# Kernel tuning notes

Measured on AMD Instinct MI355X. Metric: run time of the kernel, lower is better.

## Reference

```python
import jax, jax.numpy as jnp
import numpy as np

N_NODES = 50000
EPS = 1e-5


def setup_inputs() -> dict:
    key = jax.random.key(0)
    ks = jax.random.split(key, 8)
    B, N, F, H = 2, N_NODES, 128, 128
    E = 800000
    x = jax.random.normal(ks[0], (B, N, F), dtype=jnp.float32)
    edge_index = jax.random.randint(ks[1], (2, E), 0, N, dtype=jnp.int32)
    # Xavier-uniform weights, zero biases (matches reset_parameters)
    def xavier(k, fin, fout):
        lim = np.sqrt(6.0 / (fin + fout)).astype(np.float32)
        return jax.random.uniform(k, (fin, fout), jnp.float32, -lim, lim)
    return {
        "x": x,
        "edge_index": edge_index,
        "W1": xavier(ks[2], F, H), "b1": jnp.zeros((H,), jnp.float32),
        "W2": xavier(ks[3], H, H), "b2": jnp.zeros((H,), jnp.float32),
        "W3": xavier(ks[4], H, 1), "b3": jnp.zeros((1,), jnp.float32),
        "gamma1": jnp.ones((H,), jnp.float32), "beta1": jnp.zeros((H,), jnp.float32),
        "gamma2": jnp.ones((H,), jnp.float32), "beta2": jnp.zeros((H,), jnp.float32),
    }


def _gconv(h, edge_index, W, b):
    # h: [B, N, Fin] -> support: [B, N, Fout]
    sup = jnp.einsum('bnf,fo->bno', h, W)
    row, col = edge_index[0], edge_index[1]
    # gather source rows, scatter-add into destination rows (per batch, vmapped)
    agg = jax.vmap(lambda s: jax.ops.segment_sum(s[row], col, num_segments=N_NODES))(sup)
    return agg + b


def _bn(h, gamma, beta):
    # BatchNorm1d over flattened (B*N, F): training-mode batch statistics
    m = jnp.mean(h, axis=(0, 1))
    v = jnp.var(h, axis=(0, 1))
    return (h - m) * jax.lax.rsqrt(v + EPS) * gamma + beta


def reference(x, edge_index, W1, b1, W2, b2, W3, b3, gamma1, beta1, gamma2, beta2):
    h = _gconv(x, edge_index, W1, b1)
    h = jax.nn.relu(_bn(h, gamma1, beta1))
    h = _gconv(h, edge_index, W2, b2)
    h = jax.nn.relu(_bn(h, gamma2, beta2))
    out = _gconv(h, edge_index, W3, b3)
    return out[..., 0]  # squeeze(-1) -> [B, N]
```

## Files before the change

### kernel.cpp

```cpp
#include <hip/hip_runtime.h>

#define N_NODES 50000
#define N_EDGES 800000
#define FDIM 128
#define NROWS 100000
#define BN_EPS 1e-5f
#define CAP 64
#define NREP 64

typedef unsigned short ushort_t;
typedef unsigned int uint_t;
typedef __attribute__((ext_vector_type(8))) short bf16x8;
typedef __attribute__((ext_vector_type(4))) float f32x4;

__device__ inline ushort_t f2bf(float f) {
    uint_t x = __float_as_uint(f);
    x += 0x7fffu + ((x >> 16) & 1u);
    return (ushort_t)(x >> 16);
}
__device__ inline float4 bf4_to_f4(ushort4 u) {
    float4 f;
    f.x = __uint_as_float((uint_t)u.x << 16);
    f.y = __uint_as_float((uint_t)u.y << 16);
    f.z = __uint_as_float((uint_t)u.z << 16);
    f.w = __uint_as_float((uint_t)u.w << 16);
    return f;
}
__device__ inline void round4(float4 v, bf16x8& hi, int base) {
    hi[base + 0] = (short)f2bf(v.x);
    hi[base + 1] = (short)f2bf(v.y);
    hi[base + 2] = (short)f2bf(v.z);
    hi[base + 3] = (short)f2bf(v.w);
}

__global__ __launch_bounds__(256) void wsplit_kernel(const float* __restrict__ W1,
                                                     const float* __restrict__ W2,
                                                     ushort_t* __restrict__ wt,
                                                     int* __restrict__ cnt,
                                                     float* __restrict__ stats) {
    int idx = blockIdx.x * 256 + threadIdx.x;
    for (int i = idx; i < N_NODES; i += 32768) cnt[i] = 0;
    stats[idx] = 0.f;
    int which = idx >> 14;
    int e = idx & 16383;
    int k = e >> 7, n = e & 127;
    float f = (which ? W2 : W1)[e];
    ushort_t h = f2bf(f);
    float fh = __uint_as_float((uint_t)h << 16);
    ushort_t l = f2bf(f - fh);
    size_t base = (size_t)which * 32768;
    wt[base + n * 128 + k] = h;
    wt[base + 16384 + n * 128 + k] = l;
}

__global__ __launch_bounds__(256) void bucket_kernel(const int* __restrict__ row,
                                                     const int* __restrict__ col,
                                                     int* __restrict__ cnt,
                                                     int* __restrict__ srcbuf) {
    int e = blockIdx.x * 256 + threadIdx.x;
    if (e < N_EDGES) {
        int c = col[e];
        int p = atomicAdd(&cnt[c], 1);
        if (p < CAP) srcbuf[(c << 6) + p] = row[e];
    }
}

template <bool BN>
__global__ __launch_bounds__(256) void gemm_mfma2(const float* __restrict__ A,
                                                  const ushort_t* __restrict__ wt,
                                                  const float* __restrict__ stats,
                                                  const float* __restrict__ gamma,
                                                  const float* __restrict__ beta,
                                                  ushort_t* __restrict__ C) {
    __shared__ short lds[24576];
    __shared__ float cs[256];
    int tid = threadIdx.x;
    long r0 = (long)blockIdx.x * 64;
    const float4* A4 = (const float4*)A;

    if (BN) {
        if (tid < 128) {
            float s = 0.f, s2 = 0.f;
            for (int r = 0; r < NREP; ++r) {
                s  += stats[r * 256 + tid];
                s2 += stats[r * 256 + 128 + tid];
            }
            float inv = 1.0f / (float)NROWS;
            float mean = s * inv;
            float var = s2 * inv - mean * mean;
            float scale = gamma[tid] / sqrtf(var + BN_EPS);
            cs[tid] = scale;
            cs[128 + tid] = beta[tid] - mean * scale;
        }
        __syncthreads();
    }
    const float4* coef4 = (const float4*)cs;

    #pragma unroll
    for (int i = 0; i < 4; ++i) {
        int li = tid + i * 256;
        int r = li >> 4, j = li & 15;
        long gr = r0 + r;
        float4 va = make_float4(0.f, 0.f, 0.f, 0.f), vb = va;
        if (gr < NROWS) { va = A4[gr * 32 + j * 2]; vb = A4[gr * 32 + j * 2 + 1]; }
        if (BN) {
            float4 sc = coef4[j * 2], sh = coef4[32 + j * 2];
            va.x = fmaxf(va.x * sc.x + sh.x, 0.f);
            va.y = fmaxf(va.y * sc.y + sh.y, 0.f);
            va.z = fmaxf(va.z * sc.z + sh.z, 0.f);
            va.w = fmaxf(va.w * sc.w + sh.w, 0.f);
            sc = coef4[j * 2 + 1]; sh = coef4[32 + j * 2 + 1];
            vb.x = fmaxf(vb.x * sc.x + sh.x, 0.f);
            vb.y = fmaxf(vb.y * sc.y + sh.y, 0.f);
            vb.z = fmaxf(vb.z * sc.z + sh.z, 0.f);
            vb.w = fmaxf(vb.w * sc.w + sh.w, 0.f);
        }
        bf16x8 vh;
        round4(va, vh, 0);
        round4(vb, vh, 4);
        *(bf16x8*)&lds[r * 128 + ((j ^ (r & 15)) * 8)] = vh;
    }

    int w = tid >> 6, l = tid & 63;
    int m = l & 15, q = l >> 4;
    for (int half = 0; half < 2; ++half) {
        __syncthreads();
        #pragma unroll
        for (int i = 0; i < 8; ++i) {
            int li = tid + i * 256;
            int p = li >> 10;
            int rest = li & 1023;
            int nl = rest >> 4, j = rest & 15;
            bf16x8 v = *(const bf16x8*)&wt[(size_t)p * 16384 + (half * 64 + nl) * 128 + j * 8];
            *(bf16x8*)&lds[8192 + p * 8192 + nl * 128 + ((j ^ (nl & 15)) * 8)] = v;
        }
        __syncthreads();

        f32x4 acc[4] = {};
        #pragma unroll
        for (int s = 0; s < 4; ++s) {
            int x = (s * 4 + q) ^ m;
            bf16x8 ah = *(const bf16x8*)&lds[(w * 16 + m) * 128 + x * 8];
            #pragma unroll
            for (int c = 0; c < 4; ++c) {
                int boff = 8192 + (c * 16 + m) * 128 + x * 8;
                bf16x8 bh = *(const bf16x8*)&lds[boff];
                bf16x8 bl = *(const bf16x8*)&lds[8192 + boff];
                acc[c] = __builtin_amdgcn_mfma_f32_16x16x32_bf16(ah, bl, acc[c], 0, 0, 0);
                acc[c] = __builtin_amdgcn_mfma_f32_16x16x32_bf16(ah, bh, acc[c], 0, 0, 0);
            }
        }

        #pragma unroll
        for (int c = 0; c < 4; ++c) {
            #pragma unroll
            for (int r = 0; r < 4; ++r) {
                long gr = r0 + w * 16 + q * 4 + r;
                if (gr < NROWS) {
                    int b = gr >= N_NODES;
                    long node = gr - (long)b * N_NODES;
                    C[(node * 2 + b) * 128 + half * 64 + c * 16 + m] = f2bf(acc[c][r]);
                }
            }
        }
    }
}

__global__ __launch_bounds__(256) void aggregate_bf16(const ushort_t* __restrict__ sup,
                                                      const int* __restrict__ cnt,
                                                      const int* __restrict__ srcbuf,
                                                      float* __restrict__ agg,
                                                      float* __restrict__ stats) {
    __shared__ float lsb[4][256];
    int lane = threadIdx.x & 63;
    int wid = threadIdx.x >> 6;
    int node = blockIdx.x * 4 + wid;
    int s = lane >> 5;
    int l32 = lane & 31;
    int m = cnt[node]; if (m > CAP) m = CAP;
    const ushort4* sb = (const ushort4*)sup;
    float4 a0 = make_float4(0.f, 0.f, 0.f, 0.f);
    float4 a1 = make_float4(0.f, 0.f, 0.f, 0.f);
    int idx = (lane < m) ? srcbuf[(node << 6) + lane] : 0;
    int tmax = (m + 1) >> 1;
    #pragma unroll 2
    for (int t = 0; t < tmax; ++t) {
        int j = 2 * t + s;
        int r = __shfl(idx, j & 63);
        ushort4 u0 = sb[(size_t)r * 64 + l32];
        ushort4 u1 = sb[(size_t)r * 64 + 32 + l32];
        if (j < m) {
            float4 f0 = bf4_to_f4(u0);
            float4 f1 = bf4_to_f4(u1);
            a0.x += f0.x; a0.y += f0.y; a0.z += f0.z; a0.w += f0.w;
            a1.x += f1.x; a1.y += f1.y; a1.z += f1.z; a1.w += f1.w;
        }
    }
    a0.x += __shfl_xor(a0.x, 32); a0.y += __shfl_xor(a0.y, 32);
    a0.z += __shfl_xor(a0.z, 32); a0.w += __shfl_xor(a0.w, 32);
    a1.x += __shfl_xor(a1.x, 32); a1.y += __shfl_xor(a1.y, 32);
    a1.z += __shfl_xor(a1.z, 32); a1.w += __shfl_xor(a1.w, 32);
    float4* ag = (float4*)agg;
    if (s == 0) {
        ag[(size_t)node * 32 + l32] = a0;
        lsb[wid][l32 * 8 + 0] = a0.x + a1.x;
        lsb[wid][l32 * 8 + 1] = a0.y + a1.y;
        lsb[wid][l32 * 8 + 2] = a0.z + a1.z;
        lsb[wid][l32 * 8 + 3] = a0.w + a1.w;
        lsb[wid][l32 * 8 + 4] = a0.x * a0.x + a1.x * a1.x;
        lsb[wid][l32 * 8 + 5] = a0.y * a0.y + a1.y * a1.y;
        lsb[wid][l32 * 8 + 6] = a0.z * a0.z + a1.z * a1.z;
        lsb[wid][l32 * 8 + 7] = a0.w * a0.w + a1.w * a1.w;
    } else {
        ag[(size_t)(N_NODES + node) * 32 + l32] = a1;
    }
    __syncthreads();
    int tid = threadIdx.x;
    float v = lsb[0][tid] + lsb[1][tid] + lsb[2][tid] + lsb[3][tid];
    int f = (tid >> 3) * 4 + (tid & 3);
    int isq = (tid >> 2) & 1;
    atomicAdd(&stats[(blockIdx.x & (NREP - 1)) * 256 + isq * 128 + f], v);
}

__global__ __launch_bounds__(256) void gemv_bn_kernel(const float* __restrict__ h,
                                                      const float* __restrict__ stats,
                                                      const float* __restrict__ gamma,
                                                      const float* __restrict__ beta,
                                                      const float* __restrict__ W3,
                                                      float* __restrict__ sup3) {
    __shared__ float cs[256];
    int tid = threadIdx.x;
    if (tid < 128) {
        float s = 0.f, s2 = 0.f;
        for (int r = 0; r < NREP; ++r) {
            s  += stats[r * 256 + tid];
            s2 += stats[r * 256 + 128 + tid];
        }
        float inv = 1.0f / (float)NROWS;
        float mean = s * inv;
        float var = s2 * inv - mean * mean;
        float scale = gamma[tid] / sqrtf(var + BN_EPS);
        cs[tid] = scale;
        cs[128 + tid] = beta[tid] - mean * scale;
    }
    __syncthreads();
    int lane = tid & 63, wid = tid >> 6;
    float2 w  = ((const float2*)W3)[lane];
    float2 sc = ((const float2*)cs)[lane];
    float2 sh = ((const float2*)(cs + 128))[lane];
    #pragma unroll
    for (int r = 0; r < 4; ++r) {
        long gw = (long)blockIdx.x * 16 + wid * 4 + r;
        float2 v = ((const float2*)h)[(size_t)gw * 64 + lane];
        v.x = fmaxf(v.x * sc.x + sh.x, 0.f);
        v.y = fmaxf(v.y * sc.y + sh.y, 0.f);
        float s = v.x * w.x + v.y * w.y;
        #pragma unroll
        for (int d = 32; d > 0; d >>= 1) s += __shfl_xor(s, d);
        if (lane == 0) sup3[gw] = s;
    }
}

__global__ __launch_bounds__(256) void gather_out_kernel(const int* __restrict__ cnt,
                                                         const int* __restrict__ srcbuf,
                                                         const float* __restrict__ sup3,
                                                         const float* __restrict__ b3,
                                                         float* __restrict__ out) {
    int n = blockIdx.x * 256 + threadIdx.x;
    if (n >= N_NODES) return;
    int m = cnt[n]; if (m > CAP) m = CAP;
    int base = n << 6;
    float s0 = 0.f, s1 = 0.f;
    for (int i = 0; i < m; ++i) {
        int r = srcbuf[base + i];
        s0 += sup3[r];
        s1 += sup3[N_NODES + r];
    }
    float b = b3[0];
    out[n] = s0 + b;
    out[N_NODES + n] = s1 + b;
}


extern "C" void kernel_launch(void* const* d_in, const int* in_sizes, int n_in,
                              void* d_out, int out_size, void* d_ws, size_t ws_size,
                              hipStream_t stream) {
    const float* x      = (const float*)d_in[0];
    const int*   ei     = (const int*)d_in[1];
    const float* W1     = (const float*)d_in[2];
    const float* W2     = (const float*)d_in[4];
    const float* W3     = (const float*)d_in[6];
    const float* b3     = (const float*)d_in[7];
    const float* gamma1 = (const float*)d_in[8];
    const float* beta1  = (const float*)d_in[9];
    const float* gamma2 = (const float*)d_in[10];
    const float* beta2  = (const float*)d_in[11];
    const int* rowp = ei;
    const int* colp = ei + N_EDGES;

    ushort_t* sup   = (ushort_t*)d_ws;
    float* agg      = (float*)(sup + 12800000);
    float* sup3     = agg + 12800000;
    ushort_t* wt    = (ushort_t*)(sup3 + 100000);
    float* stats    = (float*)(wt + 65536);
    int*   cnt      = (int*)(stats + 32768);
    int*   srcbuf   = cnt + N_NODES;
    float* out      = (float*)d_out;

    wsplit_kernel  <<<128,   256, 0, stream>>>(W1, W2, wt, cnt, stats);
    bucket_kernel  <<<3125,  256, 0, stream>>>(rowp, colp, cnt, srcbuf);

    gemm_mfma2<false><<<1563,  256, 0, stream>>>(x, wt, nullptr, nullptr, nullptr, sup);
    aggregate_bf16   <<<12500, 256, 0, stream>>>(sup, cnt, srcbuf, agg, stats);

    gemm_mfma2<true> <<<1563,  256, 0, stream>>>(agg, wt + 32768, stats, gamma1, beta1, sup);
    aggregate_bf16   <<<12500, 256, 0, stream>>>(sup, cnt, srcbuf, agg, stats + 16384);

    gemv_bn_kernel   <<<6250, 256, 0, stream>>>(agg, stats + 16384, gamma2, beta2, W3, sup3);
    gather_out_kernel<<<196,  256, 0, stream>>>(cnt, srcbuf, sup3, b3, out);
}
```

Baseline: 359.1 us.

## Slice support features into 16-column planes for cache-local aggregation, shrink indices to u16

The GEMM now writes the bf16 support matrix as eight feature-slice planes of 16 columns each, instead of one 128-wide row per node. Each aggregation block handles one slice for 32 nodes, so the gathered working set per slice (about 3.2 MB) can stay cache resident rather than scattering 256-byte rows across the whole 25 MB table. Source indices are stored as 16-bit values to halve index traffic, and agg and index accesses use nontemporal hints. The cost is eight times more index reads and loop overhead per node, narrower 64-byte gathers, and a per-slice stats reduction.

```diff
diff --git a/kernel.cpp b/kernel.cpp
--- a/kernel.cpp
+++ b/kernel.cpp
@@ -12,19 +12,12 @@
 typedef unsigned int uint_t;
 typedef __attribute__((ext_vector_type(8))) short bf16x8;
 typedef __attribute__((ext_vector_type(4))) float f32x4;
+typedef __attribute__((ext_vector_type(2))) float f32x2;
 
 __device__ inline ushort_t f2bf(float f) {
     uint_t x = __float_as_uint(f);
     x += 0x7fffu + ((x >> 16) & 1u);
     return (ushort_t)(x >> 16);
-}
-__device__ inline float4 bf4_to_f4(ushort4 u) {
-    float4 f;
-    f.x = __uint_as_float((uint_t)u.x << 16);
-    f.y = __uint_as_float((uint_t)u.y << 16);
-    f.z = __uint_as_float((uint_t)u.z << 16);
-    f.w = __uint_as_float((uint_t)u.w << 16);
-    return f;
 }
 __device__ inline void round4(float4 v, bf16x8& hi, int base) {
     hi[base + 0] = (short)f2bf(v.x);
@@ -56,12 +49,12 @@
 __global__ __launch_bounds__(256) void bucket_kernel(const int* __restrict__ row,
                                                      const int* __restrict__ col,
                                                      int* __restrict__ cnt,
-                                                     int* __restrict__ srcbuf) {
+                                                     ushort_t* __restrict__ srcbuf) {
     int e = blockIdx.x * 256 + threadIdx.x;
     if (e < N_EDGES) {
         int c = col[e];
         int p = atomicAdd(&cnt[c], 1);
-        if (p < CAP) srcbuf[(c << 6) + p] = row[e];
+        if (p < CAP) srcbuf[(c << 6) + p] = (ushort_t)row[e];
     }
 }
 
@@ -159,7 +152,8 @@
                 if (gr < NROWS) {
                     int b = gr >= N_NODES;
                     long node = gr - (long)b * N_NODES;
-                    C[(node * 2 + b) * 128 + half * 64 + c * 16 + m] = f2bf(acc[c][r]);
+                    C[((size_t)(half * 4 + c) * (N_NODES * 2) + node * 2 + b) * 16 + m] =
+                        f2bf(acc[c][r]);
                 }
             }
         }
@@ -168,58 +162,76 @@
 
 __global__ __launch_bounds__(256) void aggregate_bf16(const ushort_t* __restrict__ sup,
                                                       const int* __restrict__ cnt,
-                                                      const int* __restrict__ srcbuf,
+                                                      const ushort_t* __restrict__ srcbuf,
                                                       float* __restrict__ agg,
                                                       float* __restrict__ stats) {
-    __shared__ float lsb[4][256];
-    int lane = threadIdx.x & 63;
-    int wid = threadIdx.x >> 6;
-    int node = blockIdx.x * 4 + wid;
-    int s = lane >> 5;
-    int l32 = lane & 31;
-    int m = cnt[node]; if (m > CAP) m = CAP;
-    const ushort4* sb = (const ushort4*)sup;
-    float4 a0 = make_float4(0.f, 0.f, 0.f, 0.f);
-    float4 a1 = make_float4(0.f, 0.f, 0.f, 0.f);
-    int idx = (lane < m) ? srcbuf[(node << 6) + lane] : 0;
-    int tmax = (m + 1) >> 1;
-    #pragma unroll 2
-    for (int t = 0; t < tmax; ++t) {
-        int j = 2 * t + s;
-        int r = __shfl(idx, j & 63);
-        ushort4 u0 = sb[(size_t)r * 64 + l32];
-        ushort4 u1 = sb[(size_t)r * 64 + 32 + l32];
-        if (j < m) {
-            float4 f0 = bf4_to_f4(u0);
-            float4 f1 = bf4_to_f4(u1);
-            a0.x += f0.x; a0.y += f0.y; a0.z += f0.z; a0.w += f0.w;
-            a1.x += f1.x; a1.y += f1.y; a1.z += f1.z; a1.w += f1.w;
-        }
-    }
-    a0.x += __shfl_xor(a0.x, 32); a0.y += __shfl_xor(a0.y, 32);
-    a0.z += __shfl_xor(a0.z, 32); a0.w += __shfl_xor(a0.w, 32);
-    a1.x += __shfl_xor(a1.x, 32); a1.y += __shfl_xor(a1.y, 32);
-    a1.z += __shfl_xor(a1.z, 32); a1.w += __shfl_xor(a1.w, 32);
-    float4* ag = (float4*)agg;
-    if (s == 0) {
-        ag[(size_t)node * 32 + l32] = a0;
-        lsb[wid][l32 * 8 + 0] = a0.x + a1.x;
-        lsb[wid][l32 * 8 + 1] = a0.y + a1.y;
-        lsb[wid][l32 * 8 + 2] = a0.z + a1.z;
-        lsb[wid][l32 * 8 + 3] = a0.w + a1.w;
-        lsb[wid][l32 * 8 + 4] = a0.x * a0.x + a1.x * a1.x;
-        lsb[wid][l32 * 8 + 5] = a0.y * a0.y + a1.y * a1.y;
-        lsb[wid][l32 * 8 + 6] = a0.z * a0.z + a1.z * a1.z;
-        lsb[wid][l32 * 8 + 7] = a0.w * a0.w + a1.w * a1.w;
-    } else {
-        ag[(size_t)(N_NODES + node) * 32 + l32] = a1;
+    __shared__ float lst[2][4][16];
+    int tid = threadIdx.x;
+    int lane = tid & 63, wid = tid >> 6;
+    int slice = blockIdx.x & 7;
+    int g = blockIdx.x >> 3;
+    int base_node = g * 32 + wid * 8;
+    int sub = lane & 15, eg = lane >> 4;
+    int b = sub >> 3, fpair = sub & 7;
+    const uint_t* supu = (const uint_t*)sup + (size_t)slice * N_NODES * 16;
+    f32x2* agg2 = (f32x2*)agg;
+
+    int mv = 0;
+    if (lane < 8 && base_node + lane < N_NODES) {
+        mv = cnt[base_node + lane];
+        if (mv > CAP) mv = CAP;
+    }
+    int idxv[8];
+    #pragma unroll
+    for (int k = 0; k < 8; ++k) {
+        int node = base_node + k;
+        int mk = __shfl(mv, k);
+        idxv[k] = (node < N_NODES && lane < mk)
+                    ? (int)__builtin_nontemporal_load(&srcbuf[((size_t)node << 6) + lane])
+                    : 0;
+    }
+
+    f32x2 ssum = {0.f, 0.f}, ssq = {0.f, 0.f};
+    #pragma unroll
+    for (int k = 0; k < 8; ++k) {
+        int node = base_node + k;
+        if (node < N_NODES) {
+            int mk = __shfl(mv, k);
+            float ax = 0.f, ay = 0.f;
+            int tmax = (mk + 3) >> 2;
+            #pragma unroll 2
+            for (int t = 0; t < tmax; ++t) {
+                int j = t * 4 + eg;
+                int r = __shfl(idxv[k], j & 63);
+                uint_t u = supu[(size_t)r * 16 + sub];
+                if (j < mk) {
+                    ax += __uint_as_float(u << 16);
+                    ay += __uint_as_float(u & 0xffff0000u);
+                }
+            }
+            ax += __shfl_xor(ax, 16); ay += __shfl_xor(ay, 16);
+            ax += __shfl_xor(ax, 32); ay += __shfl_xor(ay, 32);
+            if (lane < 16) {
+                size_t row = (size_t)b * N_NODES + node;
+                f32x2 v2 = {ax, ay};
+                __builtin_nontemporal_store(v2, &agg2[row * 64 + slice * 8 + fpair]);
+            }
+            float ox = __shfl_xor(ax, 8), oy = __shfl_xor(ay, 8);
+            ssum.x += ax + ox;           ssum.y += ay + oy;
+            ssq.x  += ax * ax + ox * ox; ssq.y  += ay * ay + oy * oy;
+        }
+    }
+    if (lane < 8) {
+        lst[0][wid][fpair * 2] = ssum.x; lst[0][wid][fpair * 2 + 1] = ssum.y;
+        lst[1][wid][fpair * 2] = ssq.x;  lst[1][wid][fpair * 2 + 1] = ssq.y;
     }
     __syncthreads();
-    int tid = threadIdx.x;
-    float v = lsb[0][tid] + lsb[1][tid] + lsb[2][tid] + lsb[3][tid];
-    int f = (tid >> 3) * 4 + (tid & 3);
-    int isq = (tid >> 2) & 1;
-    atomicAdd(&stats[(blockIdx.x & (NREP - 1)) * 256 + isq * 128 + f], v);
+    if (tid < 32) {
+        int which = tid >> 4, f = tid & 15;
+        float v = lst[which][0][f] + lst[which][1][f] + lst[which][2][f] + lst[which][3][f];
+        int rep = (blockIdx.x >> 3) & (NREP - 1);
+        atomicAdd(&stats[rep * 256 + which * 128 + slice * 16 + f], v);
+    }
 }
 
 __global__ __launch_bounds__(256) void gemv_bn_kernel(const float* __restrict__ h,
@@ -262,7 +274,7 @@
 }
 
 __global__ __launch_bounds__(256) void gather_out_kernel(const int* __restrict__ cnt,
-                                                         const int* __restrict__ srcbuf,
+                                                         const ushort_t* __restrict__ srcbuf,
                                                          const float* __restrict__ sup3,
                                                          const float* __restrict__ b3,
                                                          float* __restrict__ out) {
@@ -304,17 +316,17 @@
     ushort_t* wt    = (ushort_t*)(sup3 + 100000);
     float* stats    = (float*)(wt + 65536);
     int*   cnt      = (int*)(stats + 32768);
-    int*   srcbuf   = cnt + N_NODES;
+    ushort_t* srcbuf = (ushort_t*)(cnt + N_NODES);
     float* out      = (float*)d_out;
 
     wsplit_kernel  <<<128,   256, 0, stream>>>(W1, W2, wt, cnt, stats);
     bucket_kernel  <<<3125,  256, 0, stream>>>(rowp, colp, cnt, srcbuf);
 
     gemm_mfma2<false><<<1563,  256, 0, stream>>>(x, wt, nullptr, nullptr, nullptr, sup);
-    aggregate_bf16   <<<12500, 256, 0, stream>>>(sup, cnt, srcbuf, agg, stats);
+    aggregate_bf16   <<<12504, 256, 0, stream>>>(sup, cnt, srcbuf, agg, stats);
 
     gemm_mfma2<true> <<<1563,  256, 0, stream>>>(agg, wt + 32768, stats, gamma1, beta1, sup);
-    aggregate_bf16   <<<12500, 256, 0, stream>>>(sup, cnt, srcbuf, agg, stats + 16384);
+    aggregate_bf16   <<<12504, 256, 0, stream>>>(sup, cnt, srcbuf, agg, stats + 16384);
 
     gemv_bn_kernel   <<<6250, 256, 0, stream>>>(agg, stats + 16384, gamma2, beta2, W3, sup3);
     gather_out_kernel<<<196,  256, 0, stream>>>(cnt, srcbuf, sup3, b3, out);
```

After: 538.5 us. +49.9%, slower.

## Fuse init/bucket/gemm and gemv/gather into cooperative persistent kernels

Applied to the files above, without the earlier changes.

Merges the weight-split/init, edge bucketing and first GEMM into one cooperative kernel, using a grid sync after init. It likewise merges the final GEMV and output gather into a second cooperative kernel with a grid sync between them. Phases become grid-stride loops over persistent blocks, and the old separate launches remain as a fallback if the cooperative launch fails. The aim is to cut launch overhead and inter-kernel gaps, at the cost of grid.sync and fewer resident blocks for the GEMM phase.

```diff
diff --git a/kernel.cpp b/kernel.cpp
--- a/kernel.cpp
+++ b/kernel.cpp
@@ -1,12 +1,16 @@
 #include <hip/hip_runtime.h>
+#include <hip/hip_cooperative_groups.h>
+
+namespace cg = cooperative_groups;
 
 #define N_NODES 50000
 #define N_EDGES 800000
-#define FDIM 128
 #define NROWS 100000
 #define BN_EPS 1e-5f
 #define CAP 64
 #define NREP 64
+#define HEAD_BLOCKS 768
+#define TAIL_BLOCKS 1024
 
 typedef unsigned short ushort_t;
 typedef unsigned int uint_t;
@@ -33,51 +37,48 @@
     hi[base + 3] = (short)f2bf(v.w);
 }
 
-__global__ __launch_bounds__(256) void wsplit_kernel(const float* __restrict__ W1,
-                                                     const float* __restrict__ W2,
-                                                     ushort_t* __restrict__ wt,
-                                                     int* __restrict__ cnt,
-                                                     float* __restrict__ stats) {
-    int idx = blockIdx.x * 256 + threadIdx.x;
-    for (int i = idx; i < N_NODES; i += 32768) cnt[i] = 0;
-    stats[idx] = 0.f;
-    int which = idx >> 14;
-    int e = idx & 16383;
-    int k = e >> 7, n = e & 127;
-    float f = (which ? W2 : W1)[e];
-    ushort_t h = f2bf(f);
-    float fh = __uint_as_float((uint_t)h << 16);
-    ushort_t l = f2bf(f - fh);
-    size_t base = (size_t)which * 32768;
-    wt[base + n * 128 + k] = h;
-    wt[base + 16384 + n * 128 + k] = l;
-}
-
-__global__ __launch_bounds__(256) void bucket_kernel(const int* __restrict__ row,
-                                                     const int* __restrict__ col,
-                                                     int* __restrict__ cnt,
-                                                     int* __restrict__ srcbuf) {
-    int e = blockIdx.x * 256 + threadIdx.x;
-    if (e < N_EDGES) {
-        int c = col[e];
+__device__ __forceinline__ void phase_init(const float* __restrict__ W1,
+                                           const float* __restrict__ W2,
+                                           ushort_t* __restrict__ wt,
+                                           int* __restrict__ cnt,
+                                           float* __restrict__ stats,
+                                           int gtid, int gsz) {
+    for (int i = gtid; i < N_NODES; i += gsz) cnt[i] = 0;
+    if (gtid < 32768) {
+        stats[gtid] = 0.f;
+        int which = gtid >> 14;
+        int e = gtid & 16383;
+        int k = e >> 7, n = e & 127;
+        float f = (which ? W2 : W1)[e];
+        ushort_t h = f2bf(f);
+        float fh = __uint_as_float((uint_t)h << 16);
+        ushort_t l = f2bf(f - fh);
+        size_t base = (size_t)which * 32768;
+        wt[base + n * 128 + k] = h;
+        wt[base + 16384 + n * 128 + k] = l;
+    }
+}
+
+__device__ __forceinline__ void phase_bucket(const int* __restrict__ rowp,
+                                             const int* __restrict__ colp,
+                                             int* __restrict__ cnt,
+                                             int* __restrict__ srcbuf,
+                                             int gtid, int gsz) {
+    for (int e = gtid; e < N_EDGES; e += gsz) {
+        int c = colp[e];
         int p = atomicAdd(&cnt[c], 1);
-        if (p < CAP) srcbuf[(c << 6) + p] = row[e];
+        if (p < CAP) srcbuf[(c << 6) + p] = rowp[e];
     }
 }
 
 template <bool BN>
-__global__ __launch_bounds__(256) void gemm_mfma2(const float* __restrict__ A,
-                                                  const ushort_t* __restrict__ wt,
-                                                  const float* __restrict__ stats,
-                                                  const float* __restrict__ gamma,
-                                                  const float* __restrict__ beta,
-                                                  ushort_t* __restrict__ C) {
-    __shared__ short lds[24576];
-    __shared__ float cs[256];
-    int tid = threadIdx.x;
-    long r0 = (long)blockIdx.x * 64;
-    const float4* A4 = (const float4*)A;
-
+__device__ __forceinline__ void phase_gemm(const float* __restrict__ A,
+                                           const ushort_t* __restrict__ wt,
+                                           const float* __restrict__ stats,
+                                           const float* __restrict__ gamma,
+                                           const float* __restrict__ beta,
+                                           ushort_t* __restrict__ C,
+                                           short* lds, float* cs, int tid) {
     if (BN) {
         if (tid < 128) {
             float s = 0.f, s2 = 0.f;
@@ -92,78 +93,206 @@
             cs[tid] = scale;
             cs[128 + tid] = beta[tid] - mean * scale;
         }
-        __syncthreads();
-    }
+    }
+    const float4* A4 = (const float4*)A;
     const float4* coef4 = (const float4*)cs;
-
-    #pragma unroll
-    for (int i = 0; i < 4; ++i) {
-        int li = tid + i * 256;
-        int r = li >> 4, j = li & 15;
-        long gr = r0 + r;
-        float4 va = make_float4(0.f, 0.f, 0.f, 0.f), vb = va;
-        if (gr < NROWS) { va = A4[gr * 32 + j * 2]; vb = A4[gr * 32 + j * 2 + 1]; }
-        if (BN) {
-            float4 sc = coef4[j * 2], sh = coef4[32 + j * 2];
-            va.x = fmaxf(va.x * sc.x + sh.x, 0.f);
-            va.y = fmaxf(va.y * sc.y + sh.y, 0.f);
-            va.z = fmaxf(va.z * sc.z + sh.z, 0.f);
-            va.w = fmaxf(va.w * sc.w + sh.w, 0.f);
-            sc = coef4[j * 2 + 1]; sh = coef4[32 + j * 2 + 1];
-            vb.x = fmaxf(vb.x * sc.x + sh.x, 0.f);
-            vb.y = fmaxf(vb.y * sc.y + sh.y, 0.f);
-            vb.z = fmaxf(vb.z * sc.z + sh.z, 0.f);
-            vb.w = fmaxf(vb.w * sc.w + sh.w, 0.f);
-        }
-        bf16x8 vh;
-        round4(va, vh, 0);
-        round4(vb, vh, 4);
-        *(bf16x8*)&lds[r * 128 + ((j ^ (r & 15)) * 8)] = vh;
-    }
-
     int w = tid >> 6, l = tid & 63;
     int m = l & 15, q = l >> 4;
-    for (int half = 0; half < 2; ++half) {
+
+    for (int tile = blockIdx.x; tile < 1563; tile += gridDim.x) {
         __syncthreads();
+        long r0 = (long)tile * 64;
         #pragma unroll
-        for (int i = 0; i < 8; ++i) {
+        for (int i = 0; i < 4; ++i) {
             int li = tid + i * 256;
-            int p = li >> 10;
-            int rest = li & 1023;
-            int nl = rest >> 4, j = rest & 15;
-            bf16x8 v = *(const bf16x8*)&wt[(size_t)p * 16384 + (half * 64 + nl) * 128 + j * 8];
-            *(bf16x8*)&lds[8192 + p * 8192 + nl * 128 + ((j ^ (nl & 15)) * 8)] = v;
-        }
-        __syncthreads();
-
-        f32x4 acc[4] = {};
-        #pragma unroll
-        for (int s = 0; s < 4; ++s) {
-            int x = (s * 4 + q) ^ m;
-            bf16x8 ah = *(const bf16x8*)&lds[(w * 16 + m) * 128 + x * 8];
+            int r = li >> 4, j = li & 15;
+            long gr = r0 + r;
+            float4 va = make_float4(0.f, 0.f, 0.f, 0.f), vb = va;
+            if (gr < NROWS) { va = A4[gr * 32 + j * 2]; vb = A4[gr * 32 + j * 2 + 1]; }
+            if (BN) {
+                float4 sc = coef4[j * 2], sh = coef4[32 + j * 2];
+                va.x = fmaxf(va.x * sc.x + sh.x, 0.f);
+                va.y = fmaxf(va.y * sc.y + sh.y, 0.f);
+                va.z = fmaxf(va.z * sc.z + sh.z, 0.f);
+                va.w = fmaxf(va.w * sc.w + sh.w, 0.f);
+                sc = coef4[j * 2 + 1]; sh = coef4[32 + j * 2 + 1];
+                vb.x = fmaxf(vb.x * sc.x + sh.x, 0.f);
+                vb.y = fmaxf(vb.y * sc.y + sh.y, 0.f);
+                vb.z = fmaxf(vb.z * sc.z + sh.z, 0.f);
+                vb.w = fmaxf(vb.w * sc.w + sh.w, 0.f);
+            }
+            bf16x8 vh;
+            round4(va, vh, 0);
+            round4(vb, vh, 4);
+            *(bf16x8*)&lds[r * 128 + ((j ^ (r & 15)) * 8)] = vh;
+        }
+        for (int half = 0; half < 2; ++half) {
+            __syncthreads();
+            #pragma unroll
+            for (int i = 0; i < 8; ++i) {
+                int li = tid + i * 256;
+                int p = li >> 10;
+                int rest = li & 1023;
+                int nl = rest >> 4, j = rest & 15;
+                bf16x8 v = *(const bf16x8*)&wt[(size_t)p * 16384 + (half * 64 + nl) * 128 + j * 8];
+                *(bf16x8*)&lds[8192 + p * 8192 + nl * 128 + ((j ^ (nl & 15)) * 8)] = v;
+            }
+            __syncthreads();
+
+            f32x4 acc[4] = {};
+            #pragma unroll
+            for (int s = 0; s < 4; ++s) {
+                int x = (s * 4 + q) ^ m;
+                bf16x8 ah = *(const bf16x8*)&lds[(w * 16 + m) * 128 + x * 8];
+                #pragma unroll
+                for (int c = 0; c < 4; ++c) {
+                    int boff = 8192 + (c * 16 + m) * 128 + x * 8;
+                    bf16x8 bh = *(const bf16x8*)&lds[boff];
+                    bf16x8 bl = *(const bf16x8*)&lds[8192 + boff];
+                    acc[c] = __builtin_amdgcn_mfma_f32_16x16x32_bf16(ah, bl, acc[c], 0, 0, 0);
+                    acc[c] = __builtin_amdgcn_mfma_f32_16x16x32_bf16(ah, bh, acc[c], 0, 0, 0);
+                }
+            }
             #pragma unroll
             for (int c = 0; c < 4; ++c) {
-                int boff = 8192 + (c * 16 + m) * 128 + x * 8;
-                bf16x8 bh = *(const bf16x8*)&lds[boff];
-                bf16x8 bl = *(const bf16x8*)&lds[8192 + boff];
-                acc[c] = __builtin_amdgcn_mfma_f32_16x16x32_bf16(ah, bl, acc[c], 0, 0, 0);
-                acc[c] = __builtin_amdgcn_mfma_f32_16x16x32_bf16(ah, bh, acc[c], 0, 0, 0);
-            }
-        }
-
-        #pragma unroll
-        for (int c = 0; c < 4; ++c) {
-            #pragma unroll
-            for (int r = 0; r < 4; ++r) {
-                long gr = r0 + w * 16 + q * 4 + r;
-                if (gr < NROWS) {
-                    int b = gr >= N_NODES;
-                    long node = gr - (long)b * N_NODES;
-                    C[(node * 2 + b) * 128 + half * 64 + c * 16 + m] = f2bf(acc[c][r]);
+                #pragma unroll
+                for (int r = 0; r < 4; ++r) {
+                    long gr = r0 + w * 16 + q * 4 + r;
+                    if (gr < NROWS) {
+                        int b = gr >= N_NODES;
+                        long node = gr - (long)b * N_NODES;
+                        C[(node * 2 + b) * 128 + half * 64 + c * 16 + m] = f2bf(acc[c][r]);
+                    }
                 }
             }
         }
     }
+}
+
+__device__ __forceinline__ void phase_gemv(const float* __restrict__ h,
+                                           const float* __restrict__ stats,
+                                           const float* __restrict__ gamma,
+                                           const float* __restrict__ beta,
+                                           const float* __restrict__ W3,
+                                           float* __restrict__ sup3,
+                                           float* cs, int tid) {
+    if (tid < 128) {
+        float s = 0.f, s2 = 0.f;
+        for (int r = 0; r < NREP; ++r) {
+            s  += stats[r * 256 + tid];
+            s2 += stats[r * 256 + 128 + tid];
+        }
+        float inv = 1.0f / (float)NROWS;
+        float mean = s * inv;
+        float var = s2 * inv - mean * mean;
+        float scale = gamma[tid] / sqrtf(var + BN_EPS);
+        cs[tid] = scale;
+        cs[128 + tid] = beta[tid] - mean * scale;
+    }
+    __syncthreads();
+    int lane = tid & 63, wid = tid >> 6;
+    float2 w  = ((const float2*)W3)[lane];
+    float2 sc = ((const float2*)cs)[lane];
+    float2 sh = ((const float2*)(cs + 128))[lane];
+    for (int g = blockIdx.x; g < 6250; g += gridDim.x) {
+        #pragma unroll
+        for (int r = 0; r < 4; ++r) {
+            long gw = (long)g * 16 + wid * 4 + r;
+            float2 v = ((const float2*)h)[(size_t)gw * 64 + lane];
+            v.x = fmaxf(v.x * sc.x + sh.x, 0.f);
+            v.y = fmaxf(v.y * sc.y + sh.y, 0.f);
+            float s = v.x * w.x + v.y * w.y;
+            #pragma unroll
+            for (int d = 32; d > 0; d >>= 1) s += __shfl_xor(s, d);
+            if (lane == 0) sup3[gw] = s;
+        }
+    }
+}
+
+__device__ __forceinline__ void phase_gather(const int* __restrict__ cnt,
+                                             const int* __restrict__ srcbuf,
+                                             const float* __restrict__ sup3,
+                                             const float* __restrict__ b3,
+                                             float* __restrict__ out,
+                                             int gtid, int gsz) {
+    for (int n = gtid; n < N_NODES; n += gsz) {
+        int m = cnt[n]; if (m > CAP) m = CAP;
+        int base = n << 6;
+        float s0 = 0.f, s1 = 0.f;
+        for (int i = 0; i < m; ++i) {
+            int r = srcbuf[base + i];
+            s0 += sup3[r];
+            s1 += sup3[N_NODES + r];
+        }
+        float b = b3[0];
+        out[n] = s0 + b;
+        out[N_NODES + n] = s1 + b;
+    }
+}
+
+__global__ __launch_bounds__(256, 3) void fused_head(const float* __restrict__ x,
+        const int* __restrict__ ei,
+        const float* __restrict__ W1, const float* __restrict__ W2,
+        ushort_t* __restrict__ wt, int* __restrict__ cnt,
+        float* __restrict__ stats, int* __restrict__ srcbuf,
+        ushort_t* __restrict__ sup) {
+    __shared__ short lds[24576];
+    __shared__ float cs[256];
+    cg::grid_group grid = cg::this_grid();
+    int tid = threadIdx.x;
+    int gtid = blockIdx.x * 256 + tid;
+    int gsz = gridDim.x * 256;
+    phase_init(W1, W2, wt, cnt, stats, gtid, gsz);
+    grid.sync();
+    phase_bucket(ei, ei + N_EDGES, cnt, srcbuf, gtid, gsz);
+    phase_gemm<false>(x, wt, nullptr, nullptr, nullptr, sup, lds, cs, tid);
+}
+
+__global__ __launch_bounds__(256, 4) void fused_tail(const float* __restrict__ h,
+        const float* __restrict__ stats,
+        const float* __restrict__ gamma, const float* __restrict__ beta,
+        const float* __restrict__ W3, const float* __restrict__ b3,
+        float* __restrict__ sup3, const int* __restrict__ cnt,
+        const int* __restrict__ srcbuf, float* __restrict__ out) {
+    __shared__ float cs[256];
+    cg::grid_group grid = cg::this_grid();
+    int tid = threadIdx.x;
+    phase_gemv(h, stats, gamma, beta, W3, sup3, cs, tid);
+    grid.sync();
+    phase_gather(cnt, srcbuf, sup3, b3, out, blockIdx.x * 256 + tid, gridDim.x * 256);
+}
+
+__global__ __launch_bounds__(256) void k_init(const float* W1, const float* W2,
+                                              ushort_t* wt, int* cnt, float* stats) {
+    phase_init(W1, W2, wt, cnt, stats, blockIdx.x * 256 + threadIdx.x, 32768);
+}
+__global__ __launch_bounds__(256) void k_bucket(const int* rowp, const int* colp,
+                                                int* cnt, int* srcbuf) {
+    int e = blockIdx.x * 256 + threadIdx.x;
+    if (e < N_EDGES) {
+        int c = colp[e];
+        int p = atomicAdd(&cnt[c], 1);
+        if (p < CAP) srcbuf[(c << 6) + p] = rowp[e];
+    }
+}
+template <bool BN>
+__global__ __launch_bounds__(256) void k_gemm(const float* A, const ushort_t* wt,
+                                              const float* stats, const float* gamma,
+                                              const float* beta, ushort_t* C) {
+    __shared__ short lds[24576];
+    __shared__ float cs[256];
+    phase_gemm<BN>(A, wt, stats, gamma, beta, C, lds, cs, threadIdx.x);
+}
+__global__ __launch_bounds__(256) void k_gemv(const float* h, const float* stats,
+                                              const float* gamma, const float* beta,
+                                              const float* W3, float* sup3) {
+    __shared__ float cs[256];
+    phase_gemv(h, stats, gamma, beta, W3, sup3, cs, threadIdx.x);
+}
+__global__ __launch_bounds__(256) void k_gather(const int* cnt, const int* srcbuf,
+                                                const float* sup3, const float* b3,
+                                                float* out) {
+    phase_gather(cnt, srcbuf, sup3, b3, out, blockIdx.x * 256 + threadIdx.x, 50176);
 }
 
 __global__ __launch_bounds__(256) void aggregate_bf16(const ushort_t* __restrict__ sup,
@@ -222,66 +351,6 @@
     atomicAdd(&stats[(blockIdx.x & (NREP - 1)) * 256 + isq * 128 + f], v);
 }
 
-__global__ __launch_bounds__(256) void gemv_bn_kernel(const float* __restrict__ h,
-                                                      const float* __restrict__ stats,
-                                                      const float* __restrict__ gamma,
-                                                      const float* __restrict__ beta,
-                                                      const float* __restrict__ W3,
-                                                      float* __restrict__ sup3) {
-    __shared__ float cs[256];
-    int tid = threadIdx.x;
-    if (tid < 128) {
-        float s = 0.f, s2 = 0.f;
-        for (int r = 0; r < NREP; ++r) {
-            s  += stats[r * 256 + tid];
-            s2 += stats[r * 256 + 128 + tid];
-        }
-        float inv = 1.0f / (float)NROWS;
-        float mean = s * inv;
-        float var = s2 * inv - mean * mean;
-        float scale = gamma[tid] / sqrtf(var + BN_EPS);
-        cs[tid] = scale;
-        cs[128 + tid] = beta[tid] - mean * scale;
-    }
-    __syncthreads();
-    int lane = tid & 63, wid = tid >> 6;
-    float2 w  = ((const float2*)W3)[lane];
-    float2 sc = ((const float2*)cs)[lane];
-    float2 sh = ((const float2*)(cs + 128))[lane];
-    #pragma unroll
-    for (int r = 0; r < 4; ++r) {
-        long gw = (long)blockIdx.x * 16 + wid * 4 + r;
-        float2 v = ((const float2*)h)[(size_t)gw * 64 + lane];
-        v.x = fmaxf(v.x * sc.x + sh.x, 0.f);
-        v.y = fmaxf(v.y * sc.y + sh.y, 0.f);
-        float s = v.x * w.x + v.y * w.y;
-        #pragma unroll
-        for (int d = 32; d > 0; d >>= 1) s += __shfl_xor(s, d);
-        if (lane == 0) sup3[gw] = s;
-    }
-}
-
-__global__ __launch_bounds__(256) void gather_out_kernel(const int* __restrict__ cnt,
-                                                         const int* __restrict__ srcbuf,
-                                                         const float* __restrict__ sup3,
-                                                         const float* __restrict__ b3,
-                                                         float* __restrict__ out) {
-    int n = blockIdx.x * 256 + threadIdx.x;
-    if (n >= N_NODES) return;
-    int m = cnt[n]; if (m > CAP) m = CAP;
-    int base = n << 6;
-    float s0 = 0.f, s1 = 0.f;
-    for (int i = 0; i < m; ++i) {
-        int r = srcbuf[base + i];
-        s0 += sup3[r];
-        s1 += sup3[N_NODES + r];
-    }
-    float b = b3[0];
-    out[n] = s0 + b;
-    out[N_NODES + n] = s1 + b;
-}
-
-
 extern "C" void kernel_launch(void* const* d_in, const int* in_sizes, int n_in,
                               void* d_out, int out_size, void* d_ws, size_t ws_size,
                               hipStream_t stream) {
@@ -307,15 +376,31 @@
     int*   srcbuf   = cnt + N_NODES;
     float* out      = (float*)d_out;
 
-    wsplit_kernel  <<<128,   256, 0, stream>>>(W1, W2, wt, cnt, stats);
-    bucket_kernel  <<<3125,  256, 0, stream>>>(rowp, colp, cnt, srcbuf);
-
-    gemm_mfma2<false><<<1563,  256, 0, stream>>>(x, wt, nullptr, nullptr, nullptr, sup);
+    float* stats2 = stats + 16384;
+
+    void* argsA[] = { (void*)&x, (void*)&ei, (void*)&W1, (void*)&W2, (void*)&wt,
+                      (void*)&cnt, (void*)&stats, (void*)&srcbuf, (void*)&sup };
+    hipError_t errA = hipLaunchCooperativeKernel((const void*)fused_head,
+                                                 dim3(HEAD_BLOCKS), dim3(256),
+                                                 argsA, 0, stream);
+    if (errA != hipSuccess) {
+        k_init       <<<128,  256, 0, stream>>>(W1, W2, wt, cnt, stats);
+        k_bucket     <<<3125, 256, 0, stream>>>(rowp, colp, cnt, srcbuf);
+        k_gemm<false><<<1563, 256, 0, stream>>>(x, wt, nullptr, nullptr, nullptr, sup);
+    }
+
     aggregate_bf16   <<<12500, 256, 0, stream>>>(sup, cnt, srcbuf, agg, stats);
-
-    gemm_mfma2<true> <<<1563,  256, 0, stream>>>(agg, wt + 32768, stats, gamma1, beta1, sup);
-    aggregate_bf16   <<<12500, 256, 0, stream>>>(sup, cnt, srcbuf, agg, stats + 16384);
-
-    gemv_bn_kernel   <<<6250, 256, 0, stream>>>(agg, stats + 16384, gamma2, beta2, W3, sup3);
-    gather_out_kernel<<<196,  256, 0, stream>>>(cnt, srcbuf, sup3, b3, out);
-}
+    k_gemm<true>     <<<1563,  256, 0, stream>>>(agg, wt + 32768, stats, gamma1, beta1, sup);
+    aggregate_bf16   <<<12500, 256, 0, stream>>>(sup, cnt, srcbuf, agg, stats2);
+
+    void* argsB[] = { (void*)&agg, (void*)&stats2, (void*)&gamma2, (void*)&beta2,
+                      (void*)&W3, (void*)&b3, (void*)&sup3, (void*)&cnt,
+                      (void*)&srcbuf, (void*)&out };
+    hipError_t errB = hipLaunchCooperativeKernel((const void*)fused_tail,
+                                                 dim3(TAIL_BLOCKS), dim3(256),
+                                                 argsB, 0, stream);
+    if (errB != hipSuccess) {
+        k_gemv  <<<6250, 256, 0, stream>>>(agg, stats2, gamma2, beta2, W3, sup3);
+        k_gather<<<196,  256, 0, stream>>>(cnt, srcbuf, sup3, b3, out);
+    }
+}
```

New measurement: 546.7 us. 52.2% more time.

## Fuse edge bucketing into first GEMM launch and compress source indices to 16-bit

Applied to the files above, without the earlier changes.

Merges the edge-bucketing kernel and the first GEMM into one launch. Blocks are interleaved by role, one GEMM tile for every two edge chunks, so the atomic bucketing runs alongside the MFMA work and one launch boundary disappears. Source node indices in the bucket buffer are stored as 16-bit values, which halves index traffic in both aggregation passes and in the final gather. This relies on N_NODES being below 65536. The final gather now uses one thread per (node, batch) pair instead of one per node, doubling its parallelism.

```diff
diff --git a/kernel.cpp b/kernel.cpp
--- a/kernel.cpp
+++ b/kernel.cpp
@@ -2,7 +2,6 @@
 
 #define N_NODES 50000
 #define N_EDGES 800000
-#define FDIM 128
 #define NROWS 100000
 #define BN_EPS 1e-5f
 #define CAP 64
@@ -33,11 +32,11 @@
     hi[base + 3] = (short)f2bf(v.w);
 }
 
-__global__ __launch_bounds__(256) void wsplit_kernel(const float* __restrict__ W1,
-                                                     const float* __restrict__ W2,
-                                                     ushort_t* __restrict__ wt,
-                                                     int* __restrict__ cnt,
-                                                     float* __restrict__ stats) {
+__global__ __launch_bounds__(256) void k_init(const float* __restrict__ W1,
+                                              const float* __restrict__ W2,
+                                              ushort_t* __restrict__ wt,
+                                              int* __restrict__ cnt,
+                                              float* __restrict__ stats) {
     int idx = blockIdx.x * 256 + threadIdx.x;
     for (int i = idx; i < N_NODES; i += 32768) cnt[i] = 0;
     stats[idx] = 0.f;
@@ -53,29 +52,16 @@
     wt[base + 16384 + n * 128 + k] = l;
 }
 
-__global__ __launch_bounds__(256) void bucket_kernel(const int* __restrict__ row,
-                                                     const int* __restrict__ col,
-                                                     int* __restrict__ cnt,
-                                                     int* __restrict__ srcbuf) {
-    int e = blockIdx.x * 256 + threadIdx.x;
-    if (e < N_EDGES) {
-        int c = col[e];
-        int p = atomicAdd(&cnt[c], 1);
-        if (p < CAP) srcbuf[(c << 6) + p] = row[e];
-    }
-}
-
 template <bool BN>
-__global__ __launch_bounds__(256) void gemm_mfma2(const float* __restrict__ A,
-                                                  const ushort_t* __restrict__ wt,
-                                                  const float* __restrict__ stats,
-                                                  const float* __restrict__ gamma,
-                                                  const float* __restrict__ beta,
-                                                  ushort_t* __restrict__ C) {
-    __shared__ short lds[24576];
-    __shared__ float cs[256];
-    int tid = threadIdx.x;
-    long r0 = (long)blockIdx.x * 64;
+__device__ __forceinline__ void gemm_tile(int tile,
+                                          const float* __restrict__ A,
+                                          const ushort_t* __restrict__ wt,
+                                          const float* __restrict__ stats,
+                                          const float* __restrict__ gamma,
+                                          const float* __restrict__ beta,
+                                          ushort_t* __restrict__ C,
+                                          short* lds, float* cs, int tid) {
+    long r0 = (long)tile * 64;
     const float4* A4 = (const float4*)A;
 
     if (BN) {
@@ -166,9 +152,42 @@
     }
 }
 
+__global__ __launch_bounds__(256) void k_work(const float* __restrict__ x,
+                                              const int* __restrict__ rowp,
+                                              const int* __restrict__ colp,
+                                              const ushort_t* __restrict__ wt,
+                                              int* __restrict__ cnt,
+                                              ushort_t* __restrict__ srcbuf,
+                                              ushort_t* __restrict__ sup) {
+    __shared__ short lds[24576];
+    __shared__ float cs[256];
+    int b = blockIdx.x;
+    int q = b / 3, r3 = b - q * 3;
+    if (r3 == 0) {
+        gemm_tile<false>(q, x, wt, nullptr, nullptr, nullptr, sup, lds, cs, threadIdx.x);
+    } else {
+        int cid = q * 2 + (r3 - 1);
+        int e = cid * 256 + threadIdx.x;
+        int c = colp[e];
+        int p = atomicAdd(&cnt[c], 1);
+        if (p < CAP) srcbuf[(c << 6) + p] = (ushort_t)rowp[e];
+    }
+}
+
+__global__ __launch_bounds__(256) void k_gemm_bn(const float* __restrict__ A,
+                                                 const ushort_t* __restrict__ wt,
+                                                 const float* __restrict__ stats,
+                                                 const float* __restrict__ gamma,
+                                                 const float* __restrict__ beta,
+                                                 ushort_t* __restrict__ C) {
+    __shared__ short lds[24576];
+    __shared__ float cs[256];
+    gemm_tile<true>(blockIdx.x, A, wt, stats, gamma, beta, C, lds, cs, threadIdx.x);
+}
+
 __global__ __launch_bounds__(256) void aggregate_bf16(const ushort_t* __restrict__ sup,
                                                       const int* __restrict__ cnt,
-                                                      const int* __restrict__ srcbuf,
+                                                      const ushort_t* __restrict__ srcbuf,
                                                       float* __restrict__ agg,
                                                       float* __restrict__ stats) {
     __shared__ float lsb[4][256];
@@ -181,7 +200,7 @@
     const ushort4* sb = (const ushort4*)sup;
     float4 a0 = make_float4(0.f, 0.f, 0.f, 0.f);
     float4 a1 = make_float4(0.f, 0.f, 0.f, 0.f);
-    int idx = (lane < m) ? srcbuf[(node << 6) + lane] : 0;
+    int idx = (lane < m) ? (int)srcbuf[(node << 6) + lane] : 0;
     int tmax = (m + 1) >> 1;
     #pragma unroll 2
     for (int t = 0; t < tmax; ++t) {
@@ -262,25 +281,20 @@
 }
 
 __global__ __launch_bounds__(256) void gather_out_kernel(const int* __restrict__ cnt,
-                                                         const int* __restrict__ srcbuf,
+                                                         const ushort_t* __restrict__ srcbuf,
                                                          const float* __restrict__ sup3,
                                                          const float* __restrict__ b3,
                                                          float* __restrict__ out) {
-    int n = blockIdx.x * 256 + threadIdx.x;
-    if (n >= N_NODES) return;
+    int gtid = blockIdx.x * 256 + threadIdx.x;
+    if (gtid >= 2 * N_NODES) return;
+    int n = gtid >> 1, bb = gtid & 1;
     int m = cnt[n]; if (m > CAP) m = CAP;
     int base = n << 6;
-    float s0 = 0.f, s1 = 0.f;
-    for (int i = 0; i < m; ++i) {
-        int r = srcbuf[base + i];
-        s0 += sup3[r];
-        s1 += sup3[N_NODES + r];
-    }
-    float b = b3[0];
-    out[n] = s0 + b;
-    out[N_NODES + n] = s1 + b;
-}
-
+    const float* s3 = sup3 + (size_t)bb * N_NODES;
+    float s = 0.f;
+    for (int i = 0; i < m; ++i) s += s3[srcbuf[base + i]];
+    out[(size_t)bb * N_NODES + n] = s + b3[0];
+}
 
 extern "C" void kernel_launch(void* const* d_in, const int* in_sizes, int n_in,
                               void* d_out, int out_size, void* d_ws, size_t ws_size,
@@ -304,18 +318,17 @@
     ushort_t* wt    = (ushort_t*)(sup3 + 100000);
     float* stats    = (float*)(wt + 65536);
     int*   cnt      = (int*)(stats + 32768);
-    int*   srcbuf   = cnt + N_NODES;
+    ushort_t* srcbuf = (ushort_t*)(cnt + N_NODES);
     float* out      = (float*)d_out;
-
-    wsplit_kernel  <<<128,   256, 0, stream>>>(W1, W2, wt, cnt, stats);
-    bucket_kernel  <<<3125,  256, 0, stream>>>(rowp, colp, cnt, srcbuf);
-
-    gemm_mfma2<false><<<1563,  256, 0, stream>>>(x, wt, nullptr, nullptr, nullptr, sup);
-    aggregate_bf16   <<<12500, 256, 0, stream>>>(sup, cnt, srcbuf, agg, stats);
-
-    gemm_mfma2<true> <<<1563,  256, 0, stream>>>(agg, wt + 32768, stats, gamma1, beta1, sup);
-    aggregate_bf16   <<<12500, 256, 0, stream>>>(sup, cnt, srcbuf, agg, stats + 16384);
-
-    gemv_bn_kernel   <<<6250, 256, 0, stream>>>(agg, stats + 16384, gamma2, beta2, W3, sup3);
-    gather_out_kernel<<<196,  256, 0, stream>>>(cnt, srcbuf, sup3, b3, out);
-}
+    float* stats2   = stats + 16384;
+
+    k_init <<<128,  256, 0, stream>>>(W1, W2, wt, cnt, stats);
+    k_work <<<4688, 256, 0, stream>>>(x, rowp, colp, wt, cnt, srcbuf, sup);
+
+    aggregate_bf16 <<<12500, 256, 0, stream>>>(sup, cnt, srcbuf, agg, stats);
+    k_gemm_bn      <<<1563,  256, 0, stream>>>(agg, wt + 32768, stats, gamma1, beta1, sup);
+    aggregate_bf16 <<<12500, 256, 0, stream>>>(sup, cnt, srcbuf, agg, stats2);
+
+    gemv_bn_kernel   <<<6250, 256, 0, stream>>>(agg, stats2, gamma2, beta2, W3, sup3);
+    gather_out_kernel<<<391,  256, 0, stream>>>(cnt, srcbuf, sup3, b3, out);
+}
```

After: 337.3 us, median of 2. 6.1% less time.
